# Performance work log

Hardware: AMD Instinct MI355X
Metric: run time of the kernel (lower is better)

The kernel has to match this reference:

```python
import jax, jax.numpy as jnp
from jax import lax
import numpy as np

DN = ('NHWC', 'HWIO', 'NHWC')  # NHWC activations, HWIO kernels (TF layout)
EPS = 1e-3


def setup_inputs() -> dict:
    key = jax.random.key(0)
    ks = jax.random.split(key, 6)
    B, H, W, C = 16, 64, 64, 256
    x = jax.random.normal(ks[0], (B, H, W, C), jnp.float32)
    # per-sample predicted kernels (scaled to keep activations well-conditioned)
    depthwise_kernels = jax.random.normal(ks[1], (B, 3, 3, C, C), jnp.float32) * 0.02
    pointwise_kernels = jax.random.normal(ks[2], (B, 1, 1, C, C), jnp.float32) * 0.06
    biases = jax.random.normal(ks[3], (B, C), jnp.float32) * 0.1
    # shared trailing Conv2D layer params
    conv_w = jax.random.normal(ks[4], (3, 3, C, C), jnp.float32) * 0.02
    conv_b = jnp.zeros((C,), jnp.float32)
    return dict(x=x, depthwise_kernels=depthwise_kernels,
                pointwise_kernels=pointwise_kernels, biases=biases,
                conv_w=conv_w, conv_b=conv_b)


def _instance_norm(x):
    # tf.nn.moments over spatial dims (population variance), eps=0.001
    mean = jnp.mean(x, axis=(1, 2), keepdims=True)
    var = jnp.var(x, axis=(1, 2), keepdims=True)
    return (x - mean) * lax.rsqrt(var + EPS)


def _reflect_pad_hw(x, p=1):
    pad = [(0, 0)] * (x.ndim - 3) + [(p, p), (p, p), (0, 0)]
    return jnp.pad(x, pad, mode='reflect')


def _per_sample_conv(xi, dk, pk, bi):
    # xi: [H,W,C]; dk: [3,3,C,Cm]; pk: [1,1,Cm,Co]; bi: [Co]
    xp = _reflect_pad_hw(xi)[None]  # [1,H+2,W+2,C]
    y = lax.conv_general_dilated(xp, dk, (1, 1), 'VALID', dimension_numbers=DN)
    y = lax.conv_general_dilated(y, pk, (1, 1), 'VALID', dimension_numbers=DN)
    return (y + bi)[0]


def reference(x, depthwise_kernels, pointwise_kernels, biases, conv_w, conv_b):
    x = _instance_norm(x)
    # per-sample kernels -> vmap over batch (replaces tf.map_fn)
    x = jax.vmap(_per_sample_conv)(x, depthwise_kernels, pointwise_kernels, biases)
    # shared Conv2D: reflect pad + VALID conv + bias
    xp = _reflect_pad_hw(x)
    y = lax.conv_general_dilated(xp, conv_w, (1, 1), 'VALID', dimension_numbers=DN)
    return y + conv_b
```

## Files before the change

### kernel.cpp

```cpp
#include <hip/hip_runtime.h>


typedef __bf16 bf16x8 __attribute__((ext_vector_type(8)));
typedef float f32x4 __attribute__((ext_vector_type(4)));

__device__ __forceinline__ float bf2f(unsigned short v) {
    return __uint_as_float(((unsigned int)v) << 16);
}
__device__ __forceinline__ unsigned short f2bf(float f) {
    unsigned int u = __float_as_uint(f);
    unsigned int r = (u + 0x7FFFu + ((u >> 16) & 1u)) >> 16;
    return (unsigned short)r;
}
__device__ __forceinline__ float ldg_elem(const void* p, size_t idx, bool isbf) {
    return isbf ? bf2f(((const unsigned short*)p)[idx]) : ((const float*)p)[idx];
}

__device__ __forceinline__ void gload16(const void* g, void* l) {
    __builtin_amdgcn_global_load_lds(
        (__attribute__((address_space(1))) void*)(unsigned long long)g,
        (__attribute__((address_space(3))) void*)(unsigned long long)l,
        16, 0, 0);
}

#define RAW_BARRIER() do { asm volatile("" ::: "memory"); \
                           __builtin_amdgcn_s_barrier();   \
                           asm volatile("" ::: "memory"); } while (0)

__global__ void detect_dtype(const unsigned short* __restrict__ x, int* __restrict__ flag) {
    __shared__ int wild;
    if (threadIdx.x == 0) wild = 0;
    __syncthreads();
    int cnt = 0;
    for (int i = 0; i < 16; ++i) {
        float a = fabsf(bf2f(x[threadIdx.x * 16 + i]));
        if (!(a < 64.f) || (a != 0.f && a < 1e-5f)) cnt++;
    }
    atomicAdd(&wild, cnt);
    __syncthreads();
    if (threadIdx.x == 0) *flag = (wild > 512) ? 0 : 1;
}

__global__ void norm_partial2(const void* __restrict__ x, const int* __restrict__ flag,
                              float* __restrict__ partS, float* __restrict__ partQ) {
    const bool isbf = (*flag != 0);
    const int b = blockIdx.x, ch = blockIdx.y;
    const int t = threadIdx.x;
    const int l = t & 63;
    const int c4 = l * 4;
    const int sp0 = t >> 6;
    const size_t base = ((size_t)(b * 4096 + ch * 128 + sp0)) * 256 + c4;
    float s[4] = {0.f, 0.f, 0.f, 0.f}, q[4] = {0.f, 0.f, 0.f, 0.f};
    if (isbf) {
        for (int i = 0; i < 32; ++i) {
            const unsigned short* p = (const unsigned short*)x + base + (size_t)i * 1024;
            ushort4 v = *(const ushort4*)p;
            float a[4] = {bf2f(v.x), bf2f(v.y), bf2f(v.z), bf2f(v.w)};
#pragma unroll
            for (int j = 0; j < 4; ++j) { s[j] += a[j]; q[j] += a[j] * a[j]; }
        }
    } else {
        for (int i = 0; i < 32; ++i) {
            float4 v = *(const float4*)((const float*)x + base + (size_t)i * 1024);
            float a[4] = {v.x, v.y, v.z, v.w};
#pragma unroll
            for (int j = 0; j < 4; ++j) { s[j] += a[j]; q[j] += a[j] * a[j]; }
        }
    }
    __shared__ float red[4][64][9];
#pragma unroll
    for (int j = 0; j < 4; ++j) { red[sp0][l][j] = s[j]; red[sp0][l][4 + j] = q[j]; }
    __syncthreads();
    if (t < 64) {
#pragma unroll
        for (int j = 0; j < 4; ++j) {
            float ss = red[0][t][j] + red[1][t][j] + red[2][t][j] + red[3][t][j];
            float qq = red[0][t][4 + j] + red[1][t][4 + j] + red[2][t][4 + j] + red[3][t][4 + j];
            int c = t * 4 + j;
            partS[(b * 32 + ch) * 256 + c] = ss;
            partQ[(b * 32 + ch) * 256 + c] = qq;
        }
    }
}

__global__ void norm_finalize2(const float* __restrict__ partS, const float* __restrict__ partQ,
                               float* __restrict__ mean, float* __restrict__ rstd) {
    const int b = blockIdx.x, c = threadIdx.x;
    float s = 0.f, q = 0.f;
    for (int k = 0; k < 32; ++k) {
        s += partS[(b * 32 + k) * 256 + c];
        q += partQ[(b * 32 + k) * 256 + c];
    }
    float m = s * (1.f / 4096.f);
    float v = q * (1.f / 4096.f) - m * m;
    mean[b * 256 + c] = m;
    rstd[b * 256 + c] = rsqrtf(v + 1e-3f);
}

__global__ void norm_apply(const void* __restrict__ x, const int* __restrict__ flag,
                           const float* __restrict__ mean, const float* __restrict__ rstd,
                           unsigned short* __restrict__ xn) {
    const bool isbf = (*flag != 0);
    size_t e = ((size_t)blockIdx.x * 256 + threadIdx.x) * 8;
    int c0 = (int)(e & 255);
    int bc = (int)(e >> 20) * 256 + c0;
    float v[8];
    if (isbf) {
        uint4 raw = *(const uint4*)((const unsigned short*)x + e);
        unsigned int rr[4] = {raw.x, raw.y, raw.z, raw.w};
#pragma unroll
        for (int i = 0; i < 4; ++i) {
            v[2 * i]     = bf2f((unsigned short)(rr[i] & 0xFFFF));
            v[2 * i + 1] = bf2f((unsigned short)(rr[i] >> 16));
        }
    } else {
        float4 f0 = *(const float4*)((const float*)x + e);
        float4 f1 = *(const float4*)((const float*)x + e + 4);
        v[0] = f0.x; v[1] = f0.y; v[2] = f0.z; v[3] = f0.w;
        v[4] = f1.x; v[5] = f1.y; v[6] = f1.z; v[7] = f1.w;
    }
    unsigned int o[4];
#pragma unroll
    for (int i = 0; i < 4; ++i) {
        unsigned short lo = f2bf((v[2 * i]     - mean[bc + 2 * i])     * rstd[bc + 2 * i]);
        unsigned short hi = f2bf((v[2 * i + 1] - mean[bc + 2 * i + 1]) * rstd[bc + 2 * i + 1]);
        o[i] = (unsigned int)lo | ((unsigned int)hi << 16);
    }
    uint4 out; out.x = o[0]; out.y = o[1]; out.z = o[2]; out.w = o[3];
    *(uint4*)(xn + e) = out;
}

template <bool SCALE>
__global__ void transpose_wk(const void* __restrict__ src, const int* __restrict__ flag,
                             unsigned short* __restrict__ dst,
                             int s_per, long dstBStride, int coStride,
                             const float* __restrict__ rstd) {
    __shared__ unsigned short tile[64][66];
    const bool isbf = (*flag != 0);
    const int sl = blockIdx.x;
    const int b = sl / s_per;
    const size_t dbase = (size_t)b * (size_t)dstBStride + (size_t)(sl % s_per) * 256;
    const int ci0 = blockIdx.y * 64, co0 = blockIdx.z * 64;
    const int t = threadIdx.x;
    const int co4 = (t & 15) * 4;
    const int r0 = t >> 4;
#pragma unroll
    for (int i = 0; i < 4; ++i) {
        int r = r0 + i * 16;
        size_t sidx = (size_t)sl * 65536 + (size_t)(ci0 + r) * 256 + co0 + co4;
        if (isbf) {
            ushort4 v = *(const ushort4*)((const unsigned short*)src + sidx);
            tile[r][co4] = v.x; tile[r][co4 + 1] = v.y;
            tile[r][co4 + 2] = v.z; tile[r][co4 + 3] = v.w;
        } else {
            float4 v = *(const float4*)((const float*)src + sidx);
            tile[r][co4] = f2bf(v.x); tile[r][co4 + 1] = f2bf(v.y);
            tile[r][co4 + 2] = f2bf(v.z); tile[r][co4 + 3] = f2bf(v.w);
        }
    }
    __syncthreads();
    const int cip = (t & 31) * 2;
    const int cob = t >> 5;
    float s0 = 1.f, s1 = 1.f;
    if (SCALE) { s0 = rstd[b * 256 + ci0 + cip]; s1 = rstd[b * 256 + ci0 + cip + 1]; }
#pragma unroll
    for (int i = 0; i < 8; ++i) {
        int co = cob + i * 8;
        unsigned short lo = tile[cip][co], hi = tile[cip + 1][co];
        if (SCALE) { lo = f2bf(bf2f(lo) * s0); hi = f2bf(bf2f(hi) * s1); }
        *(unsigned int*)(dst + dbase + (size_t)(co0 + co) * coStride + ci0 + cip) =
            (unsigned int)lo | ((unsigned int)hi << 16);
    }
}

__global__ void corr_kernel(const unsigned short* __restrict__ dkT,
                            const float* __restrict__ mean,
                            float* __restrict__ negcorr) {
    const int b = blockIdx.x;
    const int lane = threadIdx.x & 63;
    const int co = blockIdx.y * 4 + (threadIdx.x >> 6);
    const unsigned short* wp = dkT + (size_t)(b * 256 + co) * 2304;
    const float* mb = mean + b * 256;
    const int ci0 = (lane & 31) * 8;
    float4 ma = *(const float4*)(mb + ci0);
    float4 mc = *(const float4*)(mb + ci0 + 4);
    float mm[8] = {ma.x, ma.y, ma.z, ma.w, mc.x, mc.y, mc.z, mc.w};
    float sum = 0.f;
#pragma unroll
    for (int c = 0; c < 5; ++c) {
        int k = c * 512 + lane * 8;
        if (k < 2304) {
            uint4 w = *(const uint4*)(wp + k);
            unsigned int wsv[4] = {w.x, w.y, w.z, w.w};
#pragma unroll
            for (int j = 0; j < 4; ++j) {
                sum += bf2f((unsigned short)(wsv[j] & 0xFFFF)) * mm[2 * j];
                sum += bf2f((unsigned short)(wsv[j] >> 16)) * mm[2 * j + 1];
            }
        }
    }
#pragma unroll
    for (int off = 32; off > 0; off >>= 1) sum += __shfl_down(sum, off);
    if (lane == 0) negcorr[b * 256 + co] = -sum;
}

template <int KSLICES, bool PER_SAMPLE_W, int BIAS_MODE, bool IS3X3, bool OUT_F32>
__global__ __launch_bounds__(512, 2) void gemm_conv_256(const unsigned short* __restrict__ src,
                                                        const int* __restrict__ flag,
                                                        const unsigned short* __restrict__ wT,
                                                        const void* __restrict__ bias,
                                                        void* __restrict__ dst) {
    constexpr int KTOT = KSLICES * 256;
    constexpr int NKT = KTOT / 64;
    static_assert(NKT >= 2, "pipeline needs >=2 K-tiles");
    extern __shared__ unsigned short smem[];

    const int t = threadIdx.x;
    const int lane = t & 63;
    const int wave = t >> 6;
    const int wr = wave >> 2;
    const int wc = wave & 3;
    const int bid = blockIdx.x + 16 * blockIdx.z;
    const int b  = (bid & 7) + ((bid >> 3) & 1) * 8;
    const int m0 = (bid >> 4) * 256;
    const unsigned short* srcB = src + (size_t)b * (4096 * 256);
    const unsigned short* wB = wT + (PER_SAMPLE_W ? (size_t)b * 256 * KTOT : (size_t)0);
    const bool in_bf = (BIAS_MODE >= 2) ? (*flag != 0) : true;

    const int trow = t >> 3;
    const int tswz = ((t & 7) ^ (trow & 7)) << 3;
    int hU[4], wU[4];
#pragma unroll
    for (int u = 0; u < 4; ++u) {
        int m = m0 + u * 64 + trow;
        hU[u] = m >> 6; wU[u] = m & 63;
    }
    const unsigned short* gBu[4];
#pragma unroll
    for (int u = 0; u < 4; ++u)
        gBu[u] = wB + (size_t)(u * 64 + trow) * KTOT + tswz;

    f32x4 acc[8][4];
#pragma unroll
    for (int i = 0; i < 8; ++i)
#pragma unroll
        for (int j = 0; j < 4; ++j) acc[i][j] = (f32x4){0.f, 0.f, 0.f, 0.f};

    const int fr = lane & 15;
    const int quad = lane >> 4;
    const int fsw = fr & 7;
    const int ks0 = ((quad) ^ fsw) << 3;
    const int ks1 = ((quad + 4) ^ fsw) << 3;
    const int rm = wr * 128;
    const int cn = wc * 64;

#pragma unroll
    for (int kt = 0; kt < 2; ++kt) {
        const int pdh = IS3X3 ? -1 : 0;
        const int pdw = IS3X3 ? -1 : 0;
        const int pchb = (kt & 3) << 6;
        unsigned short* ldsAW = smem + kt * 32768 + wave * 512;
#pragma unroll
        for (int u = 0; u < 4; ++u) {
            int hh = hU[u] + pdh; hh = (hh < 0) ? 1 : (hh > 63 ? 62 : hh);
            int ww = wU[u] + pdw; ww = (ww < 0) ? 1 : (ww > 63 ? 62 : ww);
            gload16(srcB + (size_t)((hh << 6) + ww) * 256 + pchb + tswz, ldsAW + u * 4096);
        }
#pragma unroll
        for (int u = 0; u < 4; ++u)
            gload16(gBu[u] + (size_t)kt * 64, ldsAW + 16384 + u * 4096);
    }
    asm volatile("s_waitcnt vmcnt(8)" ::: "memory");
    RAW_BARRIER();

    bf16x8 af[4][2], bfr[4][2];
    size_t aoff[4];
    int cur_s = -1;

    for (int i = 0; i < NKT; ++i) {
        const int buf = i & 1;
        const unsigned short* As_b = smem + buf * 32768;
        const unsigned short* Bs_b = As_b + 16384;
        unsigned short* ldsAW = smem + buf * 32768 + wave * 512;
        const int kt2 = i + 2;
        const bool st = (kt2 < NKT);

#pragma unroll
        for (int m = 0; m < 4; ++m) {
            const unsigned short* rp = As_b + (rm + m * 16 + fr) * 64;
            af[m][0] = *(const bf16x8*)(rp + ks0);
            af[m][1] = *(const bf16x8*)(rp + ks1);
        }
#pragma unroll
        for (int n = 0; n < 2; ++n) {
            const unsigned short* rp = Bs_b + (cn + n * 16 + fr) * 64;
            bfr[n][0] = *(const bf16x8*)(rp + ks0);
            bfr[n][1] = *(const bf16x8*)(rp + ks1);
        }
        __builtin_amdgcn_s_setprio(1);
#pragma unroll
        for (int m = 0; m < 4; ++m)
#pragma unroll
            for (int n = 0; n < 2; ++n) {
                acc[m][n] = __builtin_amdgcn_mfma_f32_16x16x32_bf16(af[m][0], bfr[n][0], acc[m][n], 0, 0, 0);
                acc[m][n] = __builtin_amdgcn_mfma_f32_16x16x32_bf16(af[m][1], bfr[n][1], acc[m][n], 0, 0, 0);
            }
        __builtin_amdgcn_s_setprio(0);

#pragma unroll
        for (int n = 2; n < 4; ++n) {
            const unsigned short* rp = Bs_b + (cn + n * 16 + fr) * 64;
            bfr[n][0] = *(const bf16x8*)(rp + ks0);
            bfr[n][1] = *(const bf16x8*)(rp + ks1);
        }
        __builtin_amdgcn_s_setprio(1);
#pragma unroll
        for (int m = 0; m < 4; ++m)
#pragma unroll
            for (int n = 2; n < 4; ++n) {
                acc[m][n] = __builtin_amdgcn_mfma_f32_16x16x32_bf16(af[m][0], bfr[n][0], acc[m][n], 0, 0, 0);
                acc[m][n] = __builtin_amdgcn_mfma_f32_16x16x32_bf16(af[m][1], bfr[n][1], acc[m][n], 0, 0, 0);
            }
        __builtin_amdgcn_s_setprio(0);

#pragma unroll
        for (int m = 0; m < 4; ++m) {
            const unsigned short* rp = As_b + (rm + 64 + m * 16 + fr) * 64;
            af[m][0] = *(const bf16x8*)(rp + ks0);
            af[m][1] = *(const bf16x8*)(rp + ks1);
        }
        __builtin_amdgcn_s_setprio(1);
#pragma unroll
        for (int m = 0; m < 4; ++m)
#pragma unroll
            for (int n = 0; n < 4; ++n) {
                acc[4 + m][n] = __builtin_amdgcn_mfma_f32_16x16x32_bf16(af[m][0], bfr[n][0], acc[4 + m][n], 0, 0, 0);
                acc[4 + m][n] = __builtin_amdgcn_mfma_f32_16x16x32_bf16(af[m][1], bfr[n][1], acc[4 + m][n], 0, 0, 0);
            }
        __builtin_amdgcn_s_setprio(0);

        RAW_BARRIER();
        if (st) {
            if (IS3X3) {
                const int s2 = kt2 >> 2;
                if (s2 != cur_s) {
                    cur_s = s2;
                    const int dh2 = s2 / 3 - 1, dw2 = s2 % 3 - 1;
#pragma unroll
                    for (int u = 0; u < 4; ++u) {
                        int hh = hU[u] + dh2; hh = (hh < 0) ? 1 : (hh > 63 ? 62 : hh);
                        int ww = wU[u] + dw2; ww = (ww < 0) ? 1 : (ww > 63 ? 62 : ww);
                        aoff[u] = (size_t)((hh << 6) + ww) * 256 + tswz;
                    }
                }
            } else if (cur_s < 0) {
                cur_s = 0;
#pragma unroll
                for (int u = 0; u < 4; ++u)
                    aoff[u] = (size_t)((hU[u] << 6) + wU[u]) * 256 + tswz;
            }
            const int chb2 = (kt2 & 3) << 6;
#pragma unroll
            for (int u = 0; u < 4; ++u)
                gload16(srcB + aoff[u] + chb2, ldsAW + u * 4096);
#pragma unroll
            for (int u = 0; u < 4; ++u)
                gload16(gBu[u] + (size_t)kt2 * 64, ldsAW + 16384 + u * 4096);
            asm volatile("s_waitcnt vmcnt(8)" ::: "memory");
        } else if (i + 1 < NKT) {
            asm volatile("s_waitcnt vmcnt(0)" ::: "memory");
        }
        RAW_BARRIER();
    }

    const int rbase = quad * 4;
    float bv[4];
#pragma unroll
    for (int n = 0; n < 4; ++n) {
        int nn = cn + n * 16 + fr;
        if (BIAS_MODE == 2)      bv[n] = ldg_elem(bias, b * 256 + nn, in_bf);
        else if (BIAS_MODE == 3) bv[n] = ldg_elem(bias, nn, in_bf);
        else                     bv[n] = 0.f;
    }
#pragma unroll
    for (int m = 0; m < 8; ++m) {
#pragma unroll
        for (int rr = 0; rr < 4; ++rr) {
            int mm = m0 + rm + m * 16 + rbase + rr;
            size_t rowoff = ((size_t)b * 4096 + mm) * 256;
#pragma unroll
            for (int n = 0; n < 4; ++n) {
                int nn = cn + n * 16 + fr;
                float val = acc[m][n][rr] + bv[n];
                if (OUT_F32) ((float*)dst)[rowoff + nn] = val;
                else         ((unsigned short*)dst)[rowoff + nn] = f2bf(val);
            }
        }
    }
}

template <int KSLICES, bool PER_SAMPLE_W, int BIAS_MODE, bool IS3X3, bool SRC_ADAPT, bool OUT_F32>
__global__ __launch_bounds__(256) void gemm_conv(const void* __restrict__ src,
                                                 const int* __restrict__ flag,
                                                 const unsigned short* __restrict__ wT,
                                                 const void* __restrict__ bias,
                                                 void* __restrict__ dst) {
    constexpr int KTOT = KSLICES * 256;
    __shared__ unsigned short As[128][40];
    __shared__ unsigned short Bs[128][40];

    const bool in_bf = (SRC_ADAPT || BIAS_MODE >= 2) ? (*flag != 0) : true;
    const int t = threadIdx.x;
    const int b = blockIdx.z;
    const int m0 = blockIdx.x * 128;
    const int n0 = blockIdx.y * 128;
    const size_t srcOfs = (size_t)b * (4096 * 256);
    const unsigned short* wB = wT + (PER_SAMPLE_W ? (size_t)b * 256 * KTOT : (size_t)0);

    f32x4 acc[4][4];
#pragma unroll
    for (int i = 0; i < 4; ++i)
#pragma unroll
        for (int j = 0; j < 4; ++j) acc[i][j] = (f32x4){0.f, 0.f, 0.f, 0.f};

    const int lane = t & 63;
    const int wave = t >> 6;
    const int rm = (wave >> 1) * 64;
    const int cn = (wave & 1) * 64;
    const int fr = lane & 15;
    const int kg = (lane >> 4) * 8;

    for (int kk = 0; kk < KTOT / 32; ++kk) {
        const int k0 = kk * 32;
        const int s = k0 >> 8;
        const int ci0 = k0 & 255;
        const int dh = IS3X3 ? (s / 3) - 1 : 0;
        const int dw = IS3X3 ? (s % 3) - 1 : 0;
        __syncthreads();
#pragma unroll
        for (int cc = 0; cc < 2; ++cc) {
            int ch = t + cc * 256;
            int r = ch >> 2;
            int ko = (ch & 3) << 3;
            int m = m0 + r;
            int h = m >> 6, w = m & 63;
            if (IS3X3) {
                h += dh; h = (h < 0) ? 1 : (h > 63 ? 62 : h);
                w += dw; w = (w < 0) ? 1 : (w > 63 ? 62 : w);
            }
            size_t eidx = srcOfs + (size_t)((h << 6) + w) * 256 + ci0 + ko;
            if (!SRC_ADAPT || in_bf) {
                uint4 v = *(const uint4*)((const unsigned short*)src + eidx);
                *(uint4*)&As[r][ko] = v;
            } else {
                const float* sf = (const float*)src + eidx;
                float4 f0 = *(const float4*)sf;
                float4 f1 = *(const float4*)(sf + 4);
                uint4 v;
                v.x = (unsigned int)f2bf(f0.x) | ((unsigned int)f2bf(f0.y) << 16);
                v.y = (unsigned int)f2bf(f0.z) | ((unsigned int)f2bf(f0.w) << 16);
                v.z = (unsigned int)f2bf(f1.x) | ((unsigned int)f2bf(f1.y) << 16);
                v.w = (unsigned int)f2bf(f1.z) | ((unsigned int)f2bf(f1.w) << 16);
                *(uint4*)&As[r][ko] = v;
            }
        }
#pragma unroll
        for (int cc = 0; cc < 2; ++cc) {
            int ch = t + cc * 256;
            int n = ch >> 2;
            int ko = (ch & 3) << 3;
            uint4 v = *(const uint4*)(wB + (size_t)(n0 + n) * KTOT + k0 + ko);
            *(uint4*)&Bs[n][ko] = v;
        }
        __syncthreads();

        bf16x8 af[4], bfr[4];
#pragma unroll
        for (int i = 0; i < 4; ++i) af[i] = *(const bf16x8*)&As[rm + i * 16 + fr][kg];
#pragma unroll
        for (int j = 0; j < 4; ++j) bfr[j] = *(const bf16x8*)&Bs[cn + j * 16 + fr][kg];
#pragma unroll
        for (int i = 0; i < 4; ++i)
#pragma unroll
            for (int j = 0; j < 4; ++j)
                acc[i][j] = __builtin_amdgcn_mfma_f32_16x16x32_bf16(af[i], bfr[j], acc[i][j], 0, 0, 0);
    }

    const int rbase = (lane >> 4) * 4;
    const int col = lane & 15;
    float bv[4];
#pragma unroll
    for (int j = 0; j < 4; ++j) {
        int n = n0 + cn + j * 16 + col;
        if (BIAS_MODE == 1)      bv[j] = ((const float*)bias)[b * 256 + n];
        else if (BIAS_MODE == 2) bv[j] = ldg_elem(bias, b * 256 + n, in_bf);
        else if (BIAS_MODE == 3) bv[j] = ldg_elem(bias, n, in_bf);
        else                     bv[j] = 0.f;
    }
#pragma unroll
    for (int i = 0; i < 4; ++i) {
#pragma unroll
        for (int rr = 0; rr < 4; ++rr) {
            int m = m0 + rm + i * 16 + rbase + rr;
            size_t rowoff = ((size_t)b * 4096 + m) * 256;
#pragma unroll
            for (int j = 0; j < 4; ++j) {
                int n = n0 + cn + j * 16 + col;
                float val = acc[i][j][rr] + bv[j];
                if (OUT_F32) ((float*)dst)[rowoff + n] = val;
                else         ((unsigned short*)dst)[rowoff + n] = f2bf(val);
            }
        }
    }
}

extern "C" void kernel_launch(void* const* d_in, const int* in_sizes, int n_in,
                              void* d_out, int out_size, void* d_ws, size_t ws_size,
                              hipStream_t stream) {
    const void* x    = d_in[0];
    const void* dk   = d_in[1];
    const void* pk   = d_in[2];
    const void* bias = d_in[3];
    const void* cw   = d_in[4];
    const void* cb   = d_in[5];

    const size_t NEED_SMALL = 36896768u;
    const size_t NEED_BIG   = 55771136u;
    if (ws_size < NEED_SMALL) return;
    const bool big = (ws_size >= NEED_BIG);

    char* ws = (char*)d_ws;
    int*   flagp   = (int*)ws;
    float* meanp   = (float*)(ws + 1024);
    float* rstdp   = (float*)(ws + 17408);
    float* negcorr = (float*)(ws + 33792);
    unsigned short* pkT = (unsigned short*)(ws + 65536);
    unsigned short* cwT = (unsigned short*)(ws + 2162688);
    unsigned short* dkT = (unsigned short*)(ws + 3342336);
    unsigned short* xn  = (unsigned short*)(ws + 22216704);
    float* partS = (float*)(ws + 22216704);
    float* partQ = (float*)(ws + 22216704 + 524288);
    unsigned short* y2  = big ? xn : dkT;
    unsigned short* y1  = (unsigned short*)d_out;

    hipFuncSetAttribute(reinterpret_cast<const void*>(gemm_conv_256<9, true, 0, true, false>),
                        hipFuncAttributeMaxDynamicSharedMemorySize, 131072);
    hipFuncSetAttribute(reinterpret_cast<const void*>(gemm_conv_256<1, true, 2, false, false>),
                        hipFuncAttributeMaxDynamicSharedMemorySize, 131072);
    hipFuncSetAttribute(reinterpret_cast<const void*>(gemm_conv_256<9, false, 3, true, true>),
                        hipFuncAttributeMaxDynamicSharedMemorySize, 131072);

    detect_dtype<<<1, 256, 0, stream>>>((const unsigned short*)x, flagp);
    norm_partial2<<<dim3(16, 32), 256, 0, stream>>>(x, flagp, partS, partQ);
    norm_finalize2<<<16, 256, 0, stream>>>(partS, partQ, meanp, rstdp);

    transpose_wk<false><<<dim3(16, 4, 4), 256, 0, stream>>>(pk, flagp, pkT, 1, 65536L, 256, nullptr);
    transpose_wk<false><<<dim3(9, 4, 4), 256, 0, stream>>>(cw, flagp, cwT, 9, 0L, 2304, nullptr);

    if (big) {
        transpose_wk<false><<<dim3(144, 4, 4), 256, 0, stream>>>(dk, flagp, dkT, 9, 589824L, 2304, nullptr);
        norm_apply<<<8192, 256, 0, stream>>>(x, flagp, meanp, rstdp, xn);
        gemm_conv_256<9, true, 0, true, false><<<dim3(16, 1, 16), 512, 131072, stream>>>(xn, flagp, dkT, nullptr, y1);
    } else {
        transpose_wk<true><<<dim3(144, 4, 4), 256, 0, stream>>>(dk, flagp, dkT, 9, 589824L, 2304, rstdp);
        corr_kernel<<<dim3(16, 64), 256, 0, stream>>>(dkT, meanp, negcorr);
        gemm_conv<9, true, 1, true, true, false><<<dim3(32, 2, 16), 256, 0, stream>>>(x, flagp, dkT, negcorr, y1);
    }

    gemm_conv_256<1, true, 2, false, false><<<dim3(16, 1, 16), 512, 131072, stream>>>(y1, flagp, pkT, bias, y2);
    gemm_conv_256<9, false, 3, true, true><<<dim3(16, 1, 16), 512, 131072, stream>>>(y2, flagp, cwT, cb, d_out);
}
```

Baseline: 352.5 us.

## Add dedicated 3x3 conv kernel reusing a halo window tile across taps

Adds a specialized conv3x3_256 kernel that loads a 6-row input window (with reflect padding) per 64-channel group once into shared memory and reuses it across all 9 taps, double-buffering the window and the weight tiles. This replaces the generic im2col-style gemm_conv_256 for both 3x3 convolutions and is meant to cut redundant global loads of shifted input rows. In exchange it raises dynamic shared memory to 160 KB per block, which may reduce occupancy, and it relies on hand-placed vmcnt waits that must match the issued loads.

```diff
diff --git a/kernel.cpp b/kernel.cpp
--- a/kernel.cpp
+++ b/kernel.cpp
@@ -204,6 +204,196 @@
     if (lane == 0) negcorr[b * 256 + co] = -sum;
 }
 
+template <bool PER_SAMPLE_W, int BIAS_MODE, bool OUT_F32>
+__global__ __launch_bounds__(512, 2) void conv3x3_256(const unsigned short* __restrict__ src,
+                                                      const int* __restrict__ flag,
+                                                      const unsigned short* __restrict__ wT,
+                                                      const void* __restrict__ bias,
+                                                      void* __restrict__ dst) {
+    constexpr int KTOT = 2304;
+    extern __shared__ unsigned short smem[];
+
+    const int t = threadIdx.x;
+    const int lane = t & 63;
+    const int wave = t >> 6;
+    const int wr = wave >> 2;
+    const int wc = wave & 3;
+    const int bid = blockIdx.x + 16 * blockIdx.z;
+    const int b  = (bid & 7) + ((bid >> 3) & 1) * 8;
+    const int mt = bid >> 4;
+    const int m0 = mt * 256;
+    const int R0 = mt * 4;
+    const unsigned short* srcB = src + (size_t)b * (4096 * 256);
+    const unsigned short* wB = wT + (PER_SAMPLE_W ? (size_t)b * 256 * KTOT : (size_t)0);
+    const bool in_bf = (BIAS_MODE >= 2) ? (*flag != 0) : true;
+
+    const int wx = t >> 3;
+    const int wg = ((t & 7) ^ (wx & 7)) << 3;
+    int wrow[6];
+#pragma unroll
+    for (int u = 0; u < 6; ++u) {
+        int r = R0 - 1 + u;
+        wrow[u] = (r < 0) ? 1 : (r > 63 ? 62 : r);
+    }
+    const unsigned short* winsrc[6];
+#pragma unroll
+    for (int u = 0; u < 6; ++u)
+        winsrc[u] = srcB + ((size_t)wrow[u] * 64 + wx) * 256 + wg;
+    const unsigned short* bsrc = wB + (size_t)wx * KTOT + wg;
+
+    f32x4 acc[8][4];
+#pragma unroll
+    for (int i = 0; i < 8; ++i)
+#pragma unroll
+        for (int j = 0; j < 4; ++j) acc[i][j] = (f32x4){0.f, 0.f, 0.f, 0.f};
+
+    const int fr = lane & 15;
+    const int quad = lane >> 4;
+    const int fsw = fr & 7;
+    const int ksb0 = (quad ^ fsw) << 3;
+    const int ksb1 = ((quad + 4) ^ fsw) << 3;
+    const int rm = wr * 128;
+    const int cn = wc * 64;
+
+#pragma unroll
+    for (int u = 0; u < 6; ++u)
+        gload16(winsrc[u], smem + u * 4096 + wave * 512);
+#pragma unroll
+    for (int u = 0; u < 4; ++u)
+        gload16(bsrc + (size_t)u * 64 * KTOT, smem + 49152 + u * 4096 + wave * 512);
+
+    bf16x8 af[4][2], bfr[4][2];
+
+    for (int cg = 0; cg < 4; ++cg) {
+        const unsigned short* winb = smem + (cg & 1) * 24576;
+        for (int s = 0; s < 9; ++s) {
+            const int j = cg * 9 + s;
+            const int dh = s / 3 - 1;
+            const int dw = s % 3 - 1;
+
+            if (s == 6 || s == 7)      asm volatile("s_waitcnt vmcnt(2)" ::: "memory");
+            else if (s == 8)           asm volatile("s_waitcnt vmcnt(1)" ::: "memory");
+            else                       asm volatile("s_waitcnt vmcnt(0)" ::: "memory");
+            RAW_BARRIER();
+
+            if (j < 35) {
+                const int s1 = (s == 8) ? 0 : s + 1;
+                const int cg1 = (s == 8) ? cg + 1 : cg;
+                const int koff1 = s1 * 256 + cg1 * 64;
+                unsigned short* bdst = smem + 49152 + ((j + 1) & 1) * 16384 + wave * 512;
+#pragma unroll
+                for (int u = 0; u < 4; ++u)
+                    gload16(bsrc + (size_t)u * 64 * KTOT + koff1, bdst + u * 4096);
+            }
+            if (cg < 3) {
+                unsigned short* wdst = smem + ((cg + 1) & 1) * 24576 + wave * 512;
+                const int cgo = (cg + 1) * 64;
+                if (s == 5) {
+                    gload16(winsrc[0] + cgo, wdst);
+                    gload16(winsrc[1] + cgo, wdst + 4096);
+                } else if (s == 6) {
+                    gload16(winsrc[2] + cgo, wdst + 2 * 4096);
+                    gload16(winsrc[3] + cgo, wdst + 3 * 4096);
+                } else if (s == 7) {
+                    gload16(winsrc[4] + cgo, wdst + 4 * 4096);
+                } else if (s == 8) {
+                    gload16(winsrc[5] + cgo, wdst + 5 * 4096);
+                }
+            }
+
+            int aoo[4][2];
+#pragma unroll
+            for (int mi = 0; mi < 4; ++mi) {
+                int ww = mi * 16 + fr + dw;
+                ww = (ww < 0) ? 1 : (ww > 63 ? 62 : ww);
+                const int x7 = ww & 7;
+                aoo[mi][0] = ww * 64 + ((quad ^ x7) << 3);
+                aoo[mi][1] = ww * 64 + (((quad + 4) ^ x7) << 3);
+            }
+            const unsigned short* A1 = winb + (wr * 2 + 1 + dh) * 4096;
+            const unsigned short* A2 = A1 + 4096;
+            const unsigned short* Bb = smem + 49152 + (j & 1) * 16384;
+
+#pragma unroll
+            for (int mi = 0; mi < 4; ++mi) {
+                af[mi][0] = *(const bf16x8*)(A1 + aoo[mi][0]);
+                af[mi][1] = *(const bf16x8*)(A1 + aoo[mi][1]);
+            }
+#pragma unroll
+            for (int n = 0; n < 2; ++n) {
+                const unsigned short* rp = Bb + (cn + n * 16 + fr) * 64;
+                bfr[n][0] = *(const bf16x8*)(rp + ksb0);
+                bfr[n][1] = *(const bf16x8*)(rp + ksb1);
+            }
+            __builtin_amdgcn_s_setprio(1);
+#pragma unroll
+            for (int mi = 0; mi < 4; ++mi)
+#pragma unroll
+                for (int n = 0; n < 2; ++n) {
+                    acc[mi][n] = __builtin_amdgcn_mfma_f32_16x16x32_bf16(af[mi][0], bfr[n][0], acc[mi][n], 0, 0, 0);
+                    acc[mi][n] = __builtin_amdgcn_mfma_f32_16x16x32_bf16(af[mi][1], bfr[n][1], acc[mi][n], 0, 0, 0);
+                }
+            __builtin_amdgcn_s_setprio(0);
+
+#pragma unroll
+            for (int n = 2; n < 4; ++n) {
+                const unsigned short* rp = Bb + (cn + n * 16 + fr) * 64;
+                bfr[n][0] = *(const bf16x8*)(rp + ksb0);
+                bfr[n][1] = *(const bf16x8*)(rp + ksb1);
+            }
+            __builtin_amdgcn_s_setprio(1);
+#pragma unroll
+            for (int mi = 0; mi < 4; ++mi)
+#pragma unroll
+                for (int n = 2; n < 4; ++n) {
+                    acc[mi][n] = __builtin_amdgcn_mfma_f32_16x16x32_bf16(af[mi][0], bfr[n][0], acc[mi][n], 0, 0, 0);
+                    acc[mi][n] = __builtin_amdgcn_mfma_f32_16x16x32_bf16(af[mi][1], bfr[n][1], acc[mi][n], 0, 0, 0);
+                }
+            __builtin_amdgcn_s_setprio(0);
+
+#pragma unroll
+            for (int mi = 0; mi < 4; ++mi) {
+                af[mi][0] = *(const bf16x8*)(A2 + aoo[mi][0]);
+                af[mi][1] = *(const bf16x8*)(A2 + aoo[mi][1]);
+            }
+            __builtin_amdgcn_s_setprio(1);
+#pragma unroll
+            for (int mi = 0; mi < 4; ++mi)
+#pragma unroll
+                for (int n = 0; n < 4; ++n) {
+                    acc[4 + mi][n] = __builtin_amdgcn_mfma_f32_16x16x32_bf16(af[mi][0], bfr[n][0], acc[4 + mi][n], 0, 0, 0);
+                    acc[4 + mi][n] = __builtin_amdgcn_mfma_f32_16x16x32_bf16(af[mi][1], bfr[n][1], acc[4 + mi][n], 0, 0, 0);
+                }
+            __builtin_amdgcn_s_setprio(0);
+        }
+    }
+
+    const int rbase = quad * 4;
+    float bv[4];
+#pragma unroll
+    for (int n = 0; n < 4; ++n) {
+        int nn = cn + n * 16 + fr;
+        if (BIAS_MODE == 2)      bv[n] = ldg_elem(bias, b * 256 + nn, in_bf);
+        else if (BIAS_MODE == 3) bv[n] = ldg_elem(bias, nn, in_bf);
+        else                     bv[n] = 0.f;
+    }
+#pragma unroll
+    for (int m = 0; m < 8; ++m) {
+#pragma unroll
+        for (int rr = 0; rr < 4; ++rr) {
+            int mm = m0 + rm + m * 16 + rbase + rr;
+            size_t rowoff = ((size_t)b * 4096 + mm) * 256;
+#pragma unroll
+            for (int n = 0; n < 4; ++n) {
+                int nn = cn + n * 16 + fr;
+                float val = acc[m][n][rr] + bv[n];
+                if (OUT_F32) ((float*)dst)[rowoff + nn] = val;
+                else         ((unsigned short*)dst)[rowoff + nn] = f2bf(val);
+            }
+        }
+    }
+}
+
 template <int KSLICES, bool PER_SAMPLE_W, int BIAS_MODE, bool IS3X3, bool OUT_F32>
 __global__ __launch_bounds__(512, 2) void gemm_conv_256(const unsigned short* __restrict__ src,
                                                         const int* __restrict__ flag,
@@ -543,11 +733,11 @@
     unsigned short* y2  = big ? xn : dkT;
     unsigned short* y1  = (unsigned short*)d_out;
 
-    hipFuncSetAttribute(reinterpret_cast<const void*>(gemm_conv_256<9, true, 0, true, false>),
-                        hipFuncAttributeMaxDynamicSharedMemorySize, 131072);
+    hipFuncSetAttribute(reinterpret_cast<const void*>(conv3x3_256<true, 0, false>),
+                        hipFuncAttributeMaxDynamicSharedMemorySize, 163840);
+    hipFuncSetAttribute(reinterpret_cast<const void*>(conv3x3_256<false, 3, true>),
+                        hipFuncAttributeMaxDynamicSharedMemorySize, 163840);
     hipFuncSetAttribute(reinterpret_cast<const void*>(gemm_conv_256<1, true, 2, false, false>),
-                        hipFuncAttributeMaxDynamicSharedMemorySize, 131072);
-    hipFuncSetAttribute(reinterpret_cast<const void*>(gemm_conv_256<9, false, 3, true, true>),
                         hipFuncAttributeMaxDynamicSharedMemorySize, 131072);
 
     detect_dtype<<<1, 256, 0, stream>>>((const unsigned short*)x, flagp);
@@ -560,7 +750,7 @@
     if (big) {
         transpose_wk<false><<<dim3(144, 4, 4), 256, 0, stream>>>(dk, flagp, dkT, 9, 589824L, 2304, nullptr);
         norm_apply<<<8192, 256, 0, stream>>>(x, flagp, meanp, rstdp, xn);
-        gemm_conv_256<9, true, 0, true, false><<<dim3(16, 1, 16), 512, 131072, stream>>>(xn, flagp, dkT, nullptr, y1);
+        conv3x3_256<true, 0, false><<<dim3(16, 1, 16), 512, 163840, stream>>>(xn, flagp, dkT, nullptr, y1);
     } else {
         transpose_wk<true><<<dim3(144, 4, 4), 256, 0, stream>>>(dk, flagp, dkT, 9, 589824L, 2304, rstdp);
         corr_kernel<<<dim3(16, 64), 256, 0, stream>>>(dkT, meanp, negcorr);
@@ -568,5 +758,5 @@
     }
 
     gemm_conv_256<1, true, 2, false, false><<<dim3(16, 1, 16), 512, 131072, stream>>>(y1, flagp, pkT, bias, y2);
-    gemm_conv_256<9, false, 3, true, true><<<dim3(16, 1, 16), 512, 131072, stream>>>(y2, flagp, cwT, cb, d_out);
-}
+    conv3x3_256<false, 3, true><<<dim3(16, 1, 16), 512, 163840, stream>>>(y2, flagp, cwT, cb, d_out);
+}
```

Measured after the change: 332.0 us (median of 2 runs). -5.8%, faster.
